# Kernel tuning notes

Measured on AMD Instinct MI355X. Metric: run time of the kernel, lower is better.

The kernel has to match this reference:

```python
import jax, jax.numpy as jnp
import numpy as np

D_MODEL = 96
D_STATE = 4
D_INNER = 192          # ssm_ratio * d_model
DT_RANK = 6            # ceil(d_model / 16)
K = 2                  # scan directions (fwd, reversed) over concatenated rgb||e sequence
D_CONV = 3
B, H, W = 2, 64, 64


def _layernorm(x, g, b, eps=1e-5):
    mu = jnp.mean(x, axis=-1, keepdims=True)
    var = jnp.mean((x - mu) ** 2, axis=-1, keepdims=True)
    return (x - mu) * jax.lax.rsqrt(var + eps) * g + b


def _dwconv(x, w, b):
    # x: [B, C, H, W], w: [C, 1, k, k] depthwise
    y = jax.lax.conv_general_dilated(
        x, w, window_strides=(1, 1), padding='SAME',
        feature_group_count=x.shape[1],
        dimension_numbers=('NCHW', 'OIHW', 'NCHW'))
    return y + b[None, :, None, None]


def setup_inputs() -> dict:
    key = jax.random.key(0)
    ks = jax.random.split(key, 16)
    f = lambda i, shape, s=0.02: jax.random.normal(ks[i], shape, dtype=jnp.float32) * s
    # dt_projs_bias mimics inverse-softplus of dt in [1e-3, 0.1]
    dt = jnp.exp(jax.random.uniform(ks[14], (K, D_INNER)) * (np.log(0.1) - np.log(0.001)) + np.log(0.001))
    inv_dt = dt + jnp.log(-jnp.expm1(-dt))
    return {
        'x_rgb': jax.random.normal(ks[0], (B, H, W, D_MODEL), jnp.float32),
        'x_e': jax.random.normal(ks[1], (B, H, W, D_MODEL), jnp.float32),
        'in_proj_w': f(2, (D_INNER, D_MODEL)),
        'in_proj_x_w': f(3, (D_INNER, D_MODEL)),
        'conv_w': f(4, (D_INNER, 1, D_CONV, D_CONV), 0.1),
        'conv_b': jnp.zeros((D_INNER,), jnp.float32),
        'conv_x_w': f(5, (D_INNER, 1, D_CONV, D_CONV), 0.1),
        'conv_x_b': jnp.zeros((D_INNER,), jnp.float32),
        'x_proj_weight': f(6, (K, DT_RANK + 2 * D_STATE, D_INNER)),
        'dt_projs_weight': f(7, (K, D_INNER, DT_RANK), DT_RANK ** -0.5),
        'dt_projs_bias': inv_dt.astype(jnp.float32),
        'A_logs': jnp.log(jnp.tile(jnp.arange(1, D_STATE + 1, dtype=jnp.float32)[None, :], (K * D_INNER, 1))),
        'Ds': jnp.ones((K * D_INNER,), jnp.float32),
        'ln1_g': jnp.ones((D_INNER,), jnp.float32), 'ln1_b': jnp.zeros((D_INNER,), jnp.float32),
        'ln2_g': jnp.ones((D_INNER,), jnp.float32), 'ln2_b': jnp.zeros((D_INNER,), jnp.float32),
        'out_proj_w': f(8, (D_MODEL, 2 * D_INNER)),
        'fc1_w1': f(9, (D_INNER // 16, D_INNER)), 'fc1_w2': f(10, (D_INNER, D_INNER // 16)),
        'fc2_w1': f(11, (D_INNER // 16, D_INNER)), 'fc2_w2': f(12, (D_INNER, D_INNER // 16)),
    }


def _mm_ss2d(x_rgb, x_e, in_proj_w, in_proj_x_w, conv_w, conv_b, conv_x_w, conv_x_b,
             x_proj_weight, dt_projs_weight, dt_projs_bias, A_logs, Ds,
             ln1_g, ln1_b, ln2_g, ln2_b, out_proj_w, fc1_w1, fc1_w2, fc2_w1, fc2_w2):
    # input projections (no bias)
    xr = x_rgb @ in_proj_w.T                       # [B,H,W,Di]
    xe = x_e @ in_proj_x_w.T
    xr_t = jnp.transpose(xr, (0, 3, 1, 2))         # [B,Di,H,W]
    xe_t = jnp.transpose(xe, (0, 3, 1, 2))
    xr_c = jax.nn.silu(_dwconv(xr_t, conv_w, conv_b))
    xe_c = jax.nn.silu(_dwconv(xe_t, conv_x_w, conv_x_b))

    Bb, Di, Hh, Ww = xr_c.shape
    HW = Hh * Ww
    # CrossScan_multimodal: concat rgb||e along sequence; K=2 = (forward, reversed)
    seq = jnp.concatenate([xr_c.reshape(Bb, Di, HW), xe_c.reshape(Bb, Di, HW)], axis=-1)  # [B,Di,2HW]
    xs = jnp.stack([seq, seq[..., ::-1]], axis=1)  # [B,K,Di,L]

    # projections for dt, B, C
    x_dbl = jnp.einsum('bkdl,kcd->bkcl', xs, x_proj_weight)
    dts, Bs, Cs = jnp.split(x_dbl, [DT_RANK, DT_RANK + D_STATE], axis=2)  # [B,K,R,L], [B,K,N,L] x2
    dts = jnp.einsum('bkrl,kdr->bkdl', dts, dt_projs_weight)
    delta = jax.nn.softplus(dts + dt_projs_bias.reshape(1, K, Di, 1))     # [B,K,Di,L]

    A = -jnp.exp(A_logs).reshape(K, Di, D_STATE)
    dA = jnp.exp(jnp.einsum('bkdl,kdn->bkdln', delta, A))                 # decay factors
    dBu = jnp.einsum('bkdl,bknl,bkdl->bkdln', delta, Bs, xs)              # driven input

    # S6 recurrence h_l = dA_l * h_{l-1} + dBu_l via parallel associative scan over L
    def combine(c1, c2):
        a1, b1 = c1
        a2, b2 = c2
        return a1 * a2, a2 * b1 + b2
    _, h = jax.lax.associative_scan(combine, (dA, dBu), axis=3)           # [B,K,Di,L,N]
    ys = jnp.einsum('bkdln,bknl->bkdl', h, Cs) + xs * Ds.reshape(1, K, Di, 1)

    # CrossMerge_multimodal: add reversed direction back, split modalities
    y = ys[:, 0] + ys[:, 1][..., ::-1]             # [B,Di,2HW]
    y_rgb = jnp.transpose(y[..., :HW], (0, 2, 1))  # [B,HW,Di]
    y_e = jnp.transpose(y[..., HW:], (0, 2, 1))
    y_rgb = _layernorm(y_rgb, ln1_g, ln1_b).reshape(Bb, Hh, Ww, Di)
    y_e = _layernorm(y_e, ln2_g, ln2_b).reshape(Bb, Hh, Ww, Di)

    # squeeze-excitation on pre-conv projected features
    sr = jnp.mean(xr_t, axis=(2, 3))               # [B,Di]
    se = jnp.mean(xe_t, axis=(2, 3))
    ex_r = jax.nn.sigmoid(jax.nn.silu(sr @ fc1_w1.T) @ fc1_w2.T)
    ex_e = jax.nn.sigmoid(jax.nn.silu(se @ fc2_w1.T) @ fc2_w2.T)
    y_rgb = y_rgb * ex_r[:, None, None, :]
    y_e = y_e * ex_e[:, None, None, :]

    yc = jnp.concatenate([y_rgb, y_e], axis=-1)    # [B,H,W,2Di]
    return yc @ out_proj_w.T                       # [B,H,W,d_model]


def reference(x_rgb, x_e, in_proj_w, in_proj_x_w, conv_w, conv_b, conv_x_w, conv_x_b,
              x_proj_weight, dt_projs_weight, dt_projs_bias, A_logs, Ds,
              ln1_g, ln1_b, ln2_g, ln2_b, out_proj_w, fc1_w1, fc1_w2, fc2_w1, fc2_w2):
    return _mm_ss2d(x_rgb, x_e, in_proj_w, in_proj_x_w, conv_w, conv_b, conv_x_w, conv_x_b,
                    x_proj_weight, dt_projs_weight, dt_projs_bias, A_logs, Ds,
                    ln1_g, ln1_b, ln2_g, ln2_b, out_proj_w, fc1_w1, fc1_w2, fc2_w1, fc2_w2)
```

## Files before the change

### kernel.cpp

```cpp
#include <hip/hip_runtime.h>
#include <math.h>

#define B_  2
#define H_  64
#define W_  64
#define HW  4096
#define DM  96
#define DI  192
#define NS  4
#define RK  6
#define KD  2
#define LL  8192

__device__ __forceinline__ float sigmoidf_(float x){ return 1.f/(1.f+__expf(-x)); }
__device__ __forceinline__ float4 rev4(float4 v){ return make_float4(v.w,v.z,v.y,v.x); }

__global__ void k_zero(float* __restrict__ p, int n){
  int i = blockIdx.x*256 + threadIdx.x;
  if (i < n) p[i] = 0.f;
}

__global__ __launch_bounds__(256) void k_inproj(
    const float* __restrict__ xrgb, const float* __restrict__ xe,
    const float* __restrict__ wr,   const float* __restrict__ we,
    float* __restrict__ xrt, float* __restrict__ xet, float* __restrict__ sr)
{
  __shared__ float lsW[DI*100];
  __shared__ float lsum[DI];
  const int mod = blockIdx.z, b = blockIdx.y;
  const int hw0 = blockIdx.x * 64;
  const float* x  = mod ? xe  : xrgb;
  const float* Wp = mod ? we  : wr;
  float* out      = mod ? xet : xrt;
  const int tid = threadIdx.x;
  for (int t = tid; t < DI*DM; t += 256){
    int di = t / DM, kk = t - di*DM;
    lsW[di*100 + kk] = Wp[t];
  }
  if (tid < DI) lsum[tid] = 0.f;
  const int cg = tid & 31, slot = tid >> 5;
  const int r0 = slot * 8;
  const float* xb = x + ((size_t)(b*HW) + hw0 + r0)*DM;
  float acc[8][6];
  #pragma unroll
  for (int i=0;i<8;i++)
    #pragma unroll
    for (int q=0;q<6;q++) acc[i][q]=0.f;
  __syncthreads();
  for (int kk4=0; kk4<DM/4; kk4++){
    float4 xv[8];
    #pragma unroll
    for (int i=0;i<8;i++) xv[i] = *(const float4*)(xb + (size_t)i*DM + kk4*4);
    #pragma unroll
    for (int q=0;q<6;q++){
      const float4 wv = *(const float4*)(&lsW[(cg+32*q)*100 + kk4*4]);
      #pragma unroll
      for (int i=0;i<8;i++){
        acc[i][q] = fmaf(xv[i].x, wv.x, acc[i][q]);
        acc[i][q] = fmaf(xv[i].y, wv.y, acc[i][q]);
        acc[i][q] = fmaf(xv[i].z, wv.z, acc[i][q]);
        acc[i][q] = fmaf(xv[i].w, wv.w, acc[i][q]);
      }
    }
  }
  #pragma unroll
  for (int q=0;q<6;q++){
    int di = cg + 32*q;
    float* ob = out + ((size_t)(b*DI + di))*HW + hw0 + r0;
    float ps = 0.f;
    #pragma unroll
    for (int i=0;i<8;i++){ ob[i] = acc[i][q]; ps += acc[i][q]; }
    atomicAdd(&lsum[di], ps);
  }
  __syncthreads();
  if (tid < DI) atomicAdd(&sr[((size_t)mod*B_ + b)*DI + tid], lsum[tid]);
}

__global__ __launch_bounds__(256) void k_conv(
    const float* __restrict__ xrt, const float* __restrict__ xet,
    const float* __restrict__ cwr, const float* __restrict__ cbr,
    const float* __restrict__ cwe, const float* __restrict__ cbe,
    float* __restrict__ seq)
{
  const int z = blockIdx.z; const int b = z >> 1, mod = z & 1;
  const int d = blockIdx.y;
  const float* in = (mod? xet:xrt) + ((size_t)b*DI + d)*HW;
  const float* wp = (mod? cwe:cwr) + d*9;
  const float  bias = (mod? cbe:cbr)[d];
  const int hw = blockIdx.x*256 + threadIdx.x;
  const int y = hw >> 6, x = hw & 63;
  float w[9];
  #pragma unroll
  for (int i=0;i<9;i++) w[i]=wp[i];
  float acc = bias;
  #pragma unroll
  for (int dy=-1;dy<=1;dy++){
    int yy = y+dy;
    if (yy<0||yy>=H_) continue;
    #pragma unroll
    for (int dx=-1;dx<=1;dx++){
      int xx = x+dx;
      if (xx<0||xx>=W_) continue;
      acc += in[yy*W_+xx]*w[(dy+1)*3 + dx+1];
    }
  }
  float v = acc * sigmoidf_(acc);
  seq[((size_t)b*DI + d)*LL + mod*HW + hw] = v;
}

__global__ void k_se(const float* __restrict__ sr,
                     const float* __restrict__ f11, const float* __restrict__ f12,
                     const float* __restrict__ f21, const float* __restrict__ f22,
                     float* __restrict__ ex)
{
  const int b = blockIdx.x, mod = blockIdx.y;
  const float* f1 = mod? f21:f11;
  const float* f2 = mod? f22:f12;
  __shared__ float s[DI];
  __shared__ float hid[12];
  const int t = threadIdx.x;
  s[t] = sr[((size_t)mod*B_ + b)*DI + t] * (1.f/HW);
  __syncthreads();
  if (t < 12){
    float a=0.f;
    for (int dd=0; dd<DI; dd++) a += f1[t*DI+dd]*s[dd];
    hid[t] = a * sigmoidf_(a);
  }
  __syncthreads();
  float a=0.f;
  #pragma unroll
  for (int h=0; h<12; h++) a += f2[t*12+h]*hid[h];
  ex[((size_t)mod*B_ + b)*DI + t] = sigmoidf_(a);
}

__global__ __launch_bounds__(256) void k_proj(
    const float* __restrict__ seq, const float* __restrict__ xpw,
    float* __restrict__ P)
{
  __shared__ float lw[14*DI];
  __shared__ float part[3][14][66];
  const int b = blockIdx.z, k = blockIdx.y;
  const int j0 = blockIdx.x*64;
  const int tid = threadIdx.x;
  const int jl = tid & 63, dq = tid >> 6;
  const int j = j0 + jl;
  for (int t = tid; t < 14*DI; t += 256) lw[t] = xpw[(size_t)k*14*DI + t];
  __syncthreads();
  float acc[14];
  #pragma unroll
  for (int c=0;c<14;c++) acc[c]=0.f;
  const float* sp = seq + (size_t)b*DI*LL + (size_t)(dq*48)*LL + j;
  const float* lwq = lw + dq*48;
  for (int dd=0; dd<48; dd++){
    float s = sp[(size_t)dd*LL];
    #pragma unroll
    for (int cc=0; cc<14; cc++) acc[cc] = fmaf(lwq[cc*DI+dd], s, acc[cc]);
  }
  if (dq){
    #pragma unroll
    for (int cc=0; cc<14; cc++) part[dq-1][cc][jl] = acc[cc];
  }
  __syncthreads();
  if (dq == 0){
    const int bk = b*KD + k;
    float* Pb = P + (size_t)bk*14*LL;
    #pragma unroll
    for (int cc=0; cc<14; cc++){
      float v = acc[cc] + part[0][cc][jl] + part[1][cc][jl] + part[2][cc][jl];
      Pb[(size_t)cc*LL + j] = v;
    }
  }
}

#define GETC(v_, s_) ((s_)==0?(v_).x:((s_)==1?(v_).y:((s_)==2?(v_).z:(v_).w)))
#define NT8 8

template<int KDIR, bool IPOW>
__device__ __forceinline__ void scan_impl(
    const float* __restrict__ sq, const float* __restrict__ Pb,
    const float* A, const float* dwv, float bias, float Dv,
    float* __restrict__ yo, float (*wc)[4][8], int t)
{
  const int lane = t & 63, w = t >> 6;
  float cH[NS] = {0.f,0.f,0.f,0.f};

  int jn = KDIR ? (LL - 4*t - 4) : (4*t);
  float4 pf0 = *(const float4*)(Pb + 0*(size_t)LL + jn);
  float4 pf1 = *(const float4*)(Pb + 1*(size_t)LL + jn);
  float4 pf2 = *(const float4*)(Pb + 2*(size_t)LL + jn);
  float4 pf3 = *(const float4*)(Pb + 3*(size_t)LL + jn);
  float4 pf4 = *(const float4*)(Pb + 4*(size_t)LL + jn);
  float4 pf5 = *(const float4*)(Pb + 5*(size_t)LL + jn);
  float4 pfx = *(const float4*)(sq + jn);

  for (int tt=0; tt<NT8; ++tt){
    const int j0 = jn;
    float4 f0=pf0, f1=pf1, f2=pf2, f3=pf3, f4v=pf4, f5=pf5, fx=pfx;
    float4 b0 = *(const float4*)(Pb + 6*(size_t)LL + j0);
    float4 b1 = *(const float4*)(Pb + 7*(size_t)LL + j0);
    float4 b2 = *(const float4*)(Pb + 8*(size_t)LL + j0);
    float4 b3 = *(const float4*)(Pb + 9*(size_t)LL + j0);
    float4 c0 = *(const float4*)(Pb + 10*(size_t)LL + j0);
    float4 c1 = *(const float4*)(Pb + 11*(size_t)LL + j0);
    float4 c2 = *(const float4*)(Pb + 12*(size_t)LL + j0);
    float4 c3 = *(const float4*)(Pb + 13*(size_t)LL + j0);

    if (tt+1 < NT8){
      jn = KDIR ? (LL - 1024*(tt+1) - 4*t - 4) : (1024*(tt+1) + 4*t);
      pf0 = *(const float4*)(Pb + 0*(size_t)LL + jn);
      pf1 = *(const float4*)(Pb + 1*(size_t)LL + jn);
      pf2 = *(const float4*)(Pb + 2*(size_t)LL + jn);
      pf3 = *(const float4*)(Pb + 3*(size_t)LL + jn);
      pf4 = *(const float4*)(Pb + 4*(size_t)LL + jn);
      pf5 = *(const float4*)(Pb + 5*(size_t)LL + jn);
      pfx = *(const float4*)(sq + jn);
    }

    if (KDIR){
      f0=rev4(f0); f1=rev4(f1); f2=rev4(f2); f3=rev4(f3); f4v=rev4(f4v); f5=rev4(f5);
      fx=rev4(fx);
      b0=rev4(b0); b1=rev4(b1); b2=rev4(b2); b3=rev4(b3);
      c0=rev4(c0); c1=rev4(c1); c2=rev4(c2); c3=rev4(c3);
    }

    float del[4], du[4], aP0[4], aP1[4], aP2[4], aP3[4];
    #pragma unroll
    for (int i=0;i<4;i++){
      float acc = bias;
      acc = fmaf(dwv[0],GETC(f0,i),acc); acc = fmaf(dwv[1],GETC(f1,i),acc);
      acc = fmaf(dwv[2],GETC(f2,i),acc); acc = fmaf(dwv[3],GETC(f3,i),acc);
      acc = fmaf(dwv[4],GETC(f4v,i),acc); acc = fmaf(dwv[5],GETC(f5,i),acc);
      if (IPOW){
        float ex_ = __expf(acc);
        del[i] = (acc > 20.f) ? acc : __logf(1.f + ex_);
        float a0 = 1.f/(1.f + ex_);
        float a1 = a0*a0;
        aP0[i]=a0; aP1[i]=a1; aP2[i]=a1*a0; aP3[i]=a1*a1;
      } else {
        float dl = (acc > 20.f) ? acc : __logf(1.f + __expf(acc));
        del[i] = dl;
        aP0[i]=__expf(dl*A[0]); aP1[i]=__expf(dl*A[1]);
        aP2[i]=__expf(dl*A[2]); aP3[i]=__expf(dl*A[3]);
      }
      du[i]  = del[i]*GETC(fx,i);
    }

    float lA[NS][4], lH[NS][4];
    #pragma unroll
    for (int n=0;n<NS;n++){
      float rA=1.f, rH=0.f;
      #pragma unroll
      for (int i=0;i<4;i++){
        float Bi = GETC((n==0?b0:n==1?b1:n==2?b2:b3), i);
        float ai = (n==0? aP0[i] : n==1? aP1[i] : n==2? aP2[i] : aP3[i]);
        rH = fmaf(ai, rH, du[i]*Bi);
        rA *= ai;
        lA[n][i]=rA; lH[n][i]=rH;
      }
    }

    float sA[NS], sH[NS];
    #pragma unroll
    for (int n=0;n<NS;n++){ sA[n]=lA[n][3]; sH[n]=lH[n][3]; }
    #pragma unroll
    for (int s=1; s<64; s<<=1){
      float pa[NS], ph[NS];
      #pragma unroll
      for (int n=0;n<NS;n++){ pa[n]=__shfl_up(sA[n],(unsigned)s,64); ph[n]=__shfl_up(sH[n],(unsigned)s,64); }
      if (lane >= s){
        #pragma unroll
        for (int n=0;n<NS;n++){ sH[n]=fmaf(sA[n],ph[n],sH[n]); sA[n]*=pa[n]; }
      }
    }
    float eA[NS], eH[NS];
    #pragma unroll
    for (int n=0;n<NS;n++){
      float xa = __shfl_up(sA[n],1u,64), xh = __shfl_up(sH[n],1u,64);
      eA[n] = lane ? xa : 1.f;
      eH[n] = lane ? xh : 0.f;
    }

    const int buf = tt & 1;
    if (lane == 63){
      #pragma unroll
      for (int n=0;n<NS;n++){ wc[buf][w][n]=sA[n]; wc[buf][w][4+n]=sH[n]; }
    }
    __syncthreads();

    float WA[NS]={1.f,1.f,1.f,1.f}, WH[NS]={0.f,0.f,0.f,0.f};
    float TA[NS]={1.f,1.f,1.f,1.f}, TH[NS]={0.f,0.f,0.f,0.f};
    #pragma unroll
    for (int ww=0; ww<4; ww++){
      #pragma unroll
      for (int n=0;n<NS;n++){
        float qa = wc[buf][ww][n], qh = wc[buf][ww][4+n];
        if (ww < w){ WH[n]=fmaf(qa,WH[n],qh); WA[n]*=qa; }
        TH[n]=fmaf(qa,TH[n],qh); TA[n]*=qa;
      }
    }

    float PH[NS];
    #pragma unroll
    for (int n=0;n<NS;n++){
      float GH = fmaf(WA[n], cH[n], WH[n]);
      PH[n] = fmaf(eA[n], GH, eH[n]);
    }

    float yv[4];
    #pragma unroll
    for (int i=0;i<4;i++){
      float y = Dv*GETC(fx,i);
      #pragma unroll
      for (int n=0;n<NS;n++){
        float h = fmaf(lA[n][i], PH[n], lH[n][i]);
        float Ci = GETC((n==0?c0:n==1?c1:n==2?c2:c3), i);
        y = fmaf(Ci, h, y);
      }
      yv[i] = y;
    }
    float4 o = make_float4(yv[0],yv[1],yv[2],yv[3]);
    if (KDIR) o = rev4(o);
    *(float4*)(yo + j0) = o;

    #pragma unroll
    for (int n=0;n<NS;n++) cH[n] = fmaf(TA[n], cH[n], TH[n]);
  }
}

__global__ __launch_bounds__(256, 3) void k_scan(
    const float* __restrict__ seq,  const float* __restrict__ P,
    const float* __restrict__ dtw,  const float* __restrict__ dtb,
    const float* __restrict__ Alogs,const float* __restrict__ Dsp,
    float* __restrict__ y0, float* __restrict__ y1)
{
  const int gid = blockIdx.x;
  const int d = gid % DI;
  const int k = (gid / DI) % KD;
  const int b = gid / (DI*KD);
  const int t = threadIdx.x;
  const int kd = k*DI + d;
  float A[NS];
  #pragma unroll
  for (int n=0;n<NS;n++) A[n] = -__expf(Alogs[kd*NS+n]);
  float dwv[RK];
  #pragma unroll
  for (int r=0;r<RK;r++) dwv[r] = dtw[kd*RK+r];
  const float bias = dtb[kd];
  const float Dv   = Dsp[kd];
  const float* sq = seq + ((size_t)b*DI + d)*LL;
  const int bk = b*KD + k;
  const float* Pb = P + (size_t)bk*14*LL;
  float* yo = (k ? y1 : y0) + ((size_t)b*DI + d)*LL;

  __shared__ float wc[2][4][8];

  const float tol = 1e-5f;
  const bool ipow = (fabsf(A[0]+1.f)<tol) && (fabsf(A[1]+2.f)<4.f*tol)
                 && (fabsf(A[2]+3.f)<tol*8.f) && (fabsf(A[3]+4.f)<tol*8.f);

  if (ipow){
    if (k == 0) scan_impl<0,true>(sq, Pb, A, dwv, bias, Dv, yo, wc, t);
    else        scan_impl<1,true>(sq, Pb, A, dwv, bias, Dv, yo, wc, t);
  } else {
    if (k == 0) scan_impl<0,false>(sq, Pb, A, dwv, bias, Dv, yo, wc, t);
    else        scan_impl<1,false>(sq, Pb, A, dwv, bias, Dv, yo, wc, t);
  }
}

__global__ __launch_bounds__(256) void k_ln(
    const float* __restrict__ y0, const float* __restrict__ y1,
    const float* __restrict__ ln1g, const float* __restrict__ ln1b,
    const float* __restrict__ ln2g, const float* __restrict__ ln2b,
    const float* __restrict__ ex, float* __restrict__ yln)
{
  const int b  = blockIdx.y;
  const int j0 = blockIdx.x*64;
  __shared__ float v[DI][65];
  __shared__ float ps1[4][64], ps2[4][64];
  __shared__ float mu[64], rs[64];
  const int tid = threadIdx.x;
  const int jl = tid & 63, ds = tid >> 6;
  const float* p0 = y0 + (size_t)b*DI*LL + j0;
  const float* p1 = y1 + (size_t)b*DI*LL + j0;
  for (int it=0; it<48; it++){
    int d = ds*48 + it;
    v[d][jl] = p0[(size_t)d*LL + jl] + p1[(size_t)d*LL + jl];
  }
  __syncthreads();
  float s1=0.f, s2=0.f;
  for (int it=0; it<48; it++){
    float x = v[ds*48+it][jl];
    s1 += x; s2 += x*x;
  }
  ps1[ds][jl]=s1; ps2[ds][jl]=s2;
  __syncthreads();
  if (tid < 64){
    float t1 = ps1[0][tid]+ps1[1][tid]+ps1[2][tid]+ps1[3][tid];
    float t2 = ps2[0][tid]+ps2[1][tid]+ps2[2][tid]+ps2[3][tid];
    float m  = t1*(1.f/DI);
    float var= t2*(1.f/DI) - m*m;
    mu[tid]=m; rs[tid]=rsqrtf(var + 1e-5f);
  }
  __syncthreads();
  const int mod = (j0 >= HW) ? 1 : 0;
  const float* g  = mod? ln2g:ln1g;
  const float* bb = mod? ln2b:ln1b;
  const float* exm = ex + ((size_t)mod*B_ + b)*DI;
  for (int it=0; it<48; it++){
    int idx = it*256 + tid;
    int j = idx / DI;
    int d = idx - j*DI;
    float x = v[d][j];
    float o = (x - mu[j])*rs[j]*g[d] + bb[d];
    o *= exm[d];
    yln[((size_t)b*LL + j0 + j)*DI + d] = o;
  }
}

__global__ __launch_bounds__(128) void k_out(
    const float* __restrict__ yln, const float* __restrict__ Wo, float* __restrict__ out)
{
  __shared__ float lsW[DM*68];
  const int bid  = blockIdx.x;
  const int ks   = bid & 1;
  const int rg   = bid >> 1;
  const int row0 = rg * 32;
  const int b    = row0 >> 12;
  const int hw0  = row0 & (HW-1);
  const int tid  = threadIdx.x;
  const int cg = tid & 31, slot = tid >> 5;
  const int r0 = slot * 8;
  float acc[8][3];
  #pragma unroll
  for (int i=0;i<8;i++)
    #pragma unroll
    for (int q=0;q<3;q++) acc[i][q]=0.f;

  const float* xrow = yln + ((size_t)b*LL + (ks ? HW+hw0 : hw0) + r0)*DI;
  for (int c=0;c<3;c++){
    const int colbase = ks*192 + c*64;
    for (int t=tid; t<DM*64; t+=128){
      int dm = t>>6, kkl = t&63;
      lsW[dm*68 + kkl] = Wo[(size_t)dm*384 + colbase + kkl];
    }
    __syncthreads();
    const float* xb = xrow + c*64;
    for (int kk4=0; kk4<16; kk4++){
      float4 xv[8];
      #pragma unroll
      for (int i=0;i<8;i++) xv[i] = *(const float4*)(xb + (size_t)i*DI + kk4*4);
      #pragma unroll
      for (int q=0;q<3;q++){
        const float4 wv = *(const float4*)(&lsW[(cg+32*q)*68 + kk4*4]);
        #pragma unroll
        for (int i=0;i<8;i++){
          acc[i][q] = fmaf(xv[i].x, wv.x, acc[i][q]);
          acc[i][q] = fmaf(xv[i].y, wv.y, acc[i][q]);
          acc[i][q] = fmaf(xv[i].z, wv.z, acc[i][q]);
          acc[i][q] = fmaf(xv[i].w, wv.w, acc[i][q]);
        }
      }
    }
    __syncthreads();
  }
  #pragma unroll
  for (int i=0;i<8;i++){
    float* ob = out + (size_t)(row0 + r0 + i)*DM;
    #pragma unroll
    for (int q=0;q<3;q++) atomicAdd(&ob[cg + 32*q], acc[i][q]);
  }
}

extern "C" void kernel_launch(void* const* d_in, const int* in_sizes, int n_in,
                              void* d_out, int out_size, void* d_ws, size_t ws_size,
                              hipStream_t stream) {
  const float* x_rgb      = (const float*)d_in[0];
  const float* x_e        = (const float*)d_in[1];
  const float* in_proj_w  = (const float*)d_in[2];
  const float* in_proj_xw = (const float*)d_in[3];
  const float* conv_w     = (const float*)d_in[4];
  const float* conv_b     = (const float*)d_in[5];
  const float* conv_xw    = (const float*)d_in[6];
  const float* conv_xb    = (const float*)d_in[7];
  const float* xpw        = (const float*)d_in[8];
  const float* dtw        = (const float*)d_in[9];
  const float* dtb        = (const float*)d_in[10];
  const float* A_logs     = (const float*)d_in[11];
  const float* Ds         = (const float*)d_in[12];
  const float* ln1_g      = (const float*)d_in[13];
  const float* ln1_b      = (const float*)d_in[14];
  const float* ln2_g      = (const float*)d_in[15];
  const float* ln2_b      = (const float*)d_in[16];
  const float* out_proj_w = (const float*)d_in[17];
  const float* fc1_w1     = (const float*)d_in[18];
  const float* fc1_w2     = (const float*)d_in[19];
  const float* fc2_w1     = (const float*)d_in[20];
  const float* fc2_w2     = (const float*)d_in[21];

  float* ws = (float*)d_ws;
  float* xr_t = ws;
  float* xe_t = ws + 1572864;
  float* y0   = ws;
  float* seq  = ws + 3145728;
  float* yln  = seq;
  float* y1   = ws + 6291456;
  float* P    = ws + 9437184;
  float* sr   = ws + 9895936;
  float* ex   = ws + 9896704;
  float* outp = (float*)d_out;

  k_zero  <<<dim3(3), 256, 0, stream>>>(sr, 768);
  k_inproj<<<dim3(HW/64, B_, 2), 256, 0, stream>>>(x_rgb, x_e, in_proj_w, in_proj_xw, xr_t, xe_t, sr);
  k_conv  <<<dim3(HW/256, DI, B_*2), 256, 0, stream>>>(xr_t, xe_t, conv_w, conv_b, conv_xw, conv_xb, seq);
  k_se    <<<dim3(B_, 2), DI, 0, stream>>>(sr, fc1_w1, fc1_w2, fc2_w1, fc2_w2, ex);
  k_proj  <<<dim3(LL/64, KD, B_), 256, 0, stream>>>(seq, xpw, P);
  k_scan  <<<dim3(B_*KD*DI), 256, 0, stream>>>(seq, P, dtw, dtb, A_logs, Ds, y0, y1);
  k_ln    <<<dim3(LL/64, B_), 256, 0, stream>>>(y0, y1, ln1_g, ln1_b, ln2_g, ln2_b, ex, yln);
  k_zero  <<<dim3((B_*HW*DM + 255)/256), 256, 0, stream>>>(outp, B_*HW*DM);
  k_out   <<<dim3(512), 128, 0, stream>>>(yln, out_proj_w, outp);
}
```

Measured before the change: 138.7 us.

## Remove zero and SE kernels by fusing into inproj, proj and layernorm

The squeeze-excitation channel sums are now written as per-block partials instead of global atomics, which makes the sr zero kernel unnecessary. The SE MLP is recomputed inside every layernorm block from those partials, replacing the separate k_se launch. Zeroing of the output buffer is folded into k_proj. Together this drops three kernel launches, at the cost of redundant SE work and a 64-way partial reduction in each layernorm block.

```diff
diff --git a/kernel.cpp b/kernel.cpp
--- a/kernel.cpp
+++ b/kernel.cpp
@@ -15,15 +15,10 @@
 __device__ __forceinline__ float sigmoidf_(float x){ return 1.f/(1.f+__expf(-x)); }
 __device__ __forceinline__ float4 rev4(float4 v){ return make_float4(v.w,v.z,v.y,v.x); }
 
-__global__ void k_zero(float* __restrict__ p, int n){
-  int i = blockIdx.x*256 + threadIdx.x;
-  if (i < n) p[i] = 0.f;
-}
-
 __global__ __launch_bounds__(256) void k_inproj(
     const float* __restrict__ xrgb, const float* __restrict__ xe,
     const float* __restrict__ wr,   const float* __restrict__ we,
-    float* __restrict__ xrt, float* __restrict__ xet, float* __restrict__ sr)
+    float* __restrict__ xrt, float* __restrict__ xet, float* __restrict__ srp)
 {
   __shared__ float lsW[DI*100];
   __shared__ float lsum[DI];
@@ -73,7 +68,7 @@
     atomicAdd(&lsum[di], ps);
   }
   __syncthreads();
-  if (tid < DI) atomicAdd(&sr[((size_t)mod*B_ + b)*DI + tid], lsum[tid]);
+  if (tid < DI) srp[(((size_t)mod*B_ + b)*64 + blockIdx.x)*DI + tid] = lsum[tid];
 }
 
 __global__ __launch_bounds__(256) void k_conv(
@@ -108,40 +103,21 @@
   seq[((size_t)b*DI + d)*LL + mod*HW + hw] = v;
 }
 
-__global__ void k_se(const float* __restrict__ sr,
-                     const float* __restrict__ f11, const float* __restrict__ f12,
-                     const float* __restrict__ f21, const float* __restrict__ f22,
-                     float* __restrict__ ex)
-{
-  const int b = blockIdx.x, mod = blockIdx.y;
-  const float* f1 = mod? f21:f11;
-  const float* f2 = mod? f22:f12;
-  __shared__ float s[DI];
-  __shared__ float hid[12];
-  const int t = threadIdx.x;
-  s[t] = sr[((size_t)mod*B_ + b)*DI + t] * (1.f/HW);
-  __syncthreads();
-  if (t < 12){
-    float a=0.f;
-    for (int dd=0; dd<DI; dd++) a += f1[t*DI+dd]*s[dd];
-    hid[t] = a * sigmoidf_(a);
-  }
-  __syncthreads();
-  float a=0.f;
-  #pragma unroll
-  for (int h=0; h<12; h++) a += f2[t*12+h]*hid[h];
-  ex[((size_t)mod*B_ + b)*DI + t] = sigmoidf_(a);
-}
-
 __global__ __launch_bounds__(256) void k_proj(
     const float* __restrict__ seq, const float* __restrict__ xpw,
-    float* __restrict__ P)
+    float* __restrict__ P, float* __restrict__ outz)
 {
   __shared__ float lw[14*DI];
   __shared__ float part[3][14][66];
   const int b = blockIdx.z, k = blockIdx.y;
   const int j0 = blockIdx.x*64;
   const int tid = threadIdx.x;
+  {
+    const int bid = (blockIdx.z*KD + blockIdx.y)*gridDim.x + blockIdx.x;
+    float* oz = outz + (size_t)bid*1536 + tid;
+    #pragma unroll
+    for (int q=0;q<6;q++) oz[q*256] = 0.f;
+  }
   const int jl = tid & 63, dq = tid >> 6;
   const int j = j0 + jl;
   for (int t = tid; t < 14*DI; t += 256) lw[t] = xpw[(size_t)k*14*DI + t];
@@ -371,15 +347,28 @@
     const float* __restrict__ y0, const float* __restrict__ y1,
     const float* __restrict__ ln1g, const float* __restrict__ ln1b,
     const float* __restrict__ ln2g, const float* __restrict__ ln2b,
-    const float* __restrict__ ex, float* __restrict__ yln)
+    const float* __restrict__ f11, const float* __restrict__ f12,
+    const float* __restrict__ f21, const float* __restrict__ f22,
+    const float* __restrict__ srp, float* __restrict__ yln)
 {
   const int b  = blockIdx.y;
   const int j0 = blockIdx.x*64;
+  const int mod = (j0 >= HW) ? 1 : 0;
   __shared__ float v[DI][65];
   __shared__ float ps1[4][64], ps2[4][64];
   __shared__ float mu[64], rs[64];
+  __shared__ float sm[DI];
+  __shared__ float hid[12];
+  __shared__ float exs[DI];
   const int tid = threadIdx.x;
   const int jl = tid & 63, ds = tid >> 6;
+
+  if (tid < DI){
+    const float* pp = srp + ((size_t)(mod*B_ + b)*64)*DI + tid;
+    float s = 0.f;
+    for (int q=0;q<64;q++) s += pp[(size_t)q*DI];
+    sm[tid] = s * (1.f/HW);
+  }
   const float* p0 = y0 + (size_t)b*DI*LL + j0;
   const float* p1 = y1 + (size_t)b*DI*LL + j0;
   for (int it=0; it<48; it++){
@@ -387,6 +376,14 @@
     v[d][jl] = p0[(size_t)d*LL + jl] + p1[(size_t)d*LL + jl];
   }
   __syncthreads();
+
+  const float* f1 = mod? f21:f11;
+  const float* f2 = mod? f22:f12;
+  if (tid < 12){
+    float a=0.f;
+    for (int dd=0; dd<DI; dd++) a += f1[tid*DI+dd]*sm[dd];
+    hid[tid] = a * sigmoidf_(a);
+  }
   float s1=0.f, s2=0.f;
   for (int it=0; it<48; it++){
     float x = v[ds*48+it][jl];
@@ -394,6 +391,13 @@
   }
   ps1[ds][jl]=s1; ps2[ds][jl]=s2;
   __syncthreads();
+
+  if (tid < DI){
+    float a=0.f;
+    #pragma unroll
+    for (int h=0; h<12; h++) a += f2[tid*12+h]*hid[h];
+    exs[tid] = sigmoidf_(a);
+  }
   if (tid < 64){
     float t1 = ps1[0][tid]+ps1[1][tid]+ps1[2][tid]+ps1[3][tid];
     float t2 = ps2[0][tid]+ps2[1][tid]+ps2[2][tid]+ps2[3][tid];
@@ -402,17 +406,16 @@
     mu[tid]=m; rs[tid]=rsqrtf(var + 1e-5f);
   }
   __syncthreads();
-  const int mod = (j0 >= HW) ? 1 : 0;
+
   const float* g  = mod? ln2g:ln1g;
   const float* bb = mod? ln2b:ln1b;
-  const float* exm = ex + ((size_t)mod*B_ + b)*DI;
   for (int it=0; it<48; it++){
     int idx = it*256 + tid;
     int j = idx / DI;
     int d = idx - j*DI;
     float x = v[d][j];
     float o = (x - mu[j])*rs[j]*g[d] + bb[d];
-    o *= exm[d];
+    o *= exs[d];
     yln[((size_t)b*LL + j0 + j)*DI + d] = o;
   }
 }
@@ -505,17 +508,14 @@
   float* yln  = seq;
   float* y1   = ws + 6291456;
   float* P    = ws + 9437184;
-  float* sr   = ws + 9895936;
-  float* ex   = ws + 9896704;
+  float* srp  = ws + 9895936;
   float* outp = (float*)d_out;
 
-  k_zero  <<<dim3(3), 256, 0, stream>>>(sr, 768);
-  k_inproj<<<dim3(HW/64, B_, 2), 256, 0, stream>>>(x_rgb, x_e, in_proj_w, in_proj_xw, xr_t, xe_t, sr);
+  k_inproj<<<dim3(HW/64, B_, 2), 256, 0, stream>>>(x_rgb, x_e, in_proj_w, in_proj_xw, xr_t, xe_t, srp);
   k_conv  <<<dim3(HW/256, DI, B_*2), 256, 0, stream>>>(xr_t, xe_t, conv_w, conv_b, conv_xw, conv_xb, seq);
-  k_se    <<<dim3(B_, 2), DI, 0, stream>>>(sr, fc1_w1, fc1_w2, fc2_w1, fc2_w2, ex);
-  k_proj  <<<dim3(LL/64, KD, B_), 256, 0, stream>>>(seq, xpw, P);
+  k_proj  <<<dim3(LL/64, KD, B_), 256, 0, stream>>>(seq, xpw, P, outp);
   k_scan  <<<dim3(B_*KD*DI), 256, 0, stream>>>(seq, P, dtw, dtb, A_logs, Ds, y0, y1);
-  k_ln    <<<dim3(LL/64, B_), 256, 0, stream>>>(y0, y1, ln1_g, ln1_b, ln2_g, ln2_b, ex, yln);
-  k_zero  <<<dim3((B_*HW*DM + 255)/256), 256, 0, stream>>>(outp, B_*HW*DM);
+  k_ln    <<<dim3(LL/64, B_), 256, 0, stream>>>(y0, y1, ln1_g, ln1_b, ln2_g, ln2_b,
+                                                fc1_w1, fc1_w2, fc2_w1, fc2_w2, srp, yln);
   k_out   <<<dim3(512), 128, 0, stream>>>(yln, out_proj_w, outp);
 }
```

Result: faster. 130.0 us (median of 2 runs) (-6.2%).
